# Performance work log

Hardware: AMD Instinct MI355X
Metric: run time of the kernel (lower is better)

Reference implementation:

```python
import jax, jax.numpy as jnp
import numpy as np


def layer_norm(x, gamma, beta, eps=1e-6):
    # Torch module uses unbiased std (ddof=1) and divides by (std + eps)
    mean = x.mean(-1, keepdims=True)
    std = jnp.std(x, axis=-1, keepdims=True, ddof=1)
    return gamma * (x - mean) / (std + eps) + beta


def gelu_erf(x):
    return 0.5 * x * (1.0 + jax.lax.erf(x / jnp.sqrt(jnp.asarray(2.0, x.dtype))))


def setup_inputs() -> dict:
    B, S, D, H, F = 32, 512, 1024, 16, 4096
    key = jax.random.key(0)
    ks = jax.random.split(key, 16)
    w = lambda k, shp: (jax.random.normal(k, shp, jnp.float32) * 0.02)
    return {
        "x": jax.random.normal(ks[0], (B, S, D), jnp.float32),
        "mask": jax.random.randint(ks[1], (B, S), 0, 2).astype(jnp.int32),
        "adj": jax.random.normal(ks[2], (B, 1, S, S), jnp.float32) * 0.1,
        "num_head": H,
        "Wq": w(ks[3], (D, D)), "bq": jnp.zeros((D,), jnp.float32),
        "Wk": w(ks[4], (D, D)), "bk": jnp.zeros((D,), jnp.float32),
        "Wv": w(ks[5], (D, D)), "bv": jnp.zeros((D,), jnp.float32),
        "Wo": w(ks[6], (D, D)), "bo": jnp.zeros((D,), jnp.float32),
        "W1": w(ks[7], (D, F)), "b1": jnp.zeros((F,), jnp.float32),
        "W2": w(ks[8], (F, D)), "b2": jnp.zeros((D,), jnp.float32),
        "gamma": jnp.ones((D,), jnp.float32),
        "beta": jnp.zeros((D,), jnp.float32),
    }


def reference(x, mask, adj, num_head, Wq, bq, Wk, bk, Wv, bv, Wo, bo,
              W1, b1, W2, b2, gamma, beta):
    B, S, D = x.shape
    H = num_head
    dk = D // H
    split = lambda t: t.reshape(B, S, H, dk).transpose(0, 2, 1, 3)  # [B,H,S,dk]
    q = split(x @ Wq + bq)
    k = split(x @ Wk + bk)
    v = split(x @ Wv + bv)
    scores = jnp.einsum('bhqd,bhkd->bhqk', q, k) / np.float32(np.sqrt(dk))
    m = mask[:, None, None, :].astype(x.dtype)  # [B,1,1,S]
    scores = scores + m * jnp.asarray(-1e9, x.dtype) + adj
    attn = jax.nn.softmax(scores, axis=-1)
    ctx = jnp.einsum('bhqk,bhkd->bhqd', attn, v)
    ctx = ctx.transpose(0, 2, 1, 3).reshape(B, S, D)
    attn_out = ctx @ Wo + bo  # dropout is identity at eval
    out1 = layer_norm(x + attn_out, gamma, beta)
    ffn = gelu_erf(out1 @ W1 + b1) @ W2 + b2
    return layer_norm(out1 + ffn, gamma, beta)
```

## Files before the change

### kernel.cpp

```cpp
#include <hip/hip_runtime.h>
#include <stdint.h>
#include <math.h>

typedef unsigned short u16;
typedef __attribute__((ext_vector_type(8))) __bf16 bf16x8;
typedef __attribute__((ext_vector_type(4))) float f32x4;
typedef __attribute__((ext_vector_type(4))) unsigned short u16x4;

__device__ __forceinline__ float b2f(u16 u) {
    unsigned int i = ((unsigned int)u) << 16;
    float f; __builtin_memcpy(&f, &i, 4); return f;
}
__device__ __forceinline__ u16 f2b(float f) {
    unsigned int i; __builtin_memcpy(&i, &f, 4);
    i = (i + 0x7FFFu + ((i >> 16) & 1u)) >> 16;
    return (u16)i;
}
__device__ __forceinline__ bf16x8 ld8_cvt(const float* p) {
    float4 f0 = *(const float4*)p, f1 = *(const float4*)(p + 4);
    u16 t[8] = {f2b(f0.x), f2b(f0.y), f2b(f0.z), f2b(f0.w),
                f2b(f1.x), f2b(f1.y), f2b(f1.z), f2b(f1.w)};
    bf16x8 r; __builtin_memcpy(&r, t, 16); return r;
}

__global__ __launch_bounds__(256) void transpose_f32_bf16(
    const float* __restrict__ in, u16* __restrict__ out, int R, int C)
{
    __shared__ float t[32][33];
    int bx = blockIdx.x * 32, by = blockIdx.y * 32;
    int x = threadIdx.x, y = threadIdx.y;
    #pragma unroll
    for (int j = 0; j < 32; j += 8)
        t[y + j][x] = in[(size_t)(by + y + j) * C + bx + x];
    __syncthreads();
    #pragma unroll
    for (int j = 0; j < 32; j += 8)
        out[(size_t)(bx + y + j) * R + by + x] = f2b(t[x][y + j]);
}

template<int EPI, bool AF32>
__global__ __launch_bounds__(256) void gemm_bt(
    const void* __restrict__ Av, const u16* __restrict__ Bt, int N, int K,
    u16* __restrict__ C, const float* __restrict__ bias,
    u16* __restrict__ qo, u16* __restrict__ ko, u16* __restrict__ vo,
    const float* __restrict__ bq, const float* __restrict__ bk,
    const float* __restrict__ bv)
{
    __shared__ __align__(16) u16 Asm[128 * 32];
    __shared__ __align__(16) u16 Bsm[128 * 32];
    const int tid  = threadIdx.x;
    const int lane = tid & 63, wave = tid >> 6;
    const int lrow = lane & 15, quad = lane >> 4;
    const int bm = blockIdx.x * 128, bn = blockIdx.y * 128;

    const int srow = tid >> 2;
    const int skol = (tid & 3) * 8;
    const float* gAf0 = (const float*)Av + (size_t)(bm + srow) * K + skol;
    const float* gAf1 = gAf0 + (size_t)64 * K;
    const u16*   gAh0 = (const u16*)Av + (size_t)(bm + srow) * K + skol;
    const u16*   gAh1 = gAh0 + (size_t)64 * K;
    const u16*   gB0  = Bt + (size_t)(bn + srow) * K + skol;
    const u16*   gB1  = gB0 + (size_t)64 * K;

    bf16x8 ra0, ra1, rb0, rb1;
    if (AF32) { ra0 = ld8_cvt(gAf0); ra1 = ld8_cvt(gAf1); }
    else      { ra0 = *(const bf16x8*)gAh0; ra1 = *(const bf16x8*)gAh1; }
    rb0 = *(const bf16x8*)gB0;
    rb1 = *(const bf16x8*)gB1;

    const int wm = wave >> 1, wn = wave & 1;
    f32x4 acc[4][4] = {};

    for (int kt = 0; kt < K; kt += 32) {
        __syncthreads();
        *(bf16x8*)&Asm[(size_t)tid * 8]         = ra0;
        *(bf16x8*)&Asm[((size_t)tid + 256) * 8] = ra1;
        *(bf16x8*)&Bsm[(size_t)tid * 8]         = rb0;
        *(bf16x8*)&Bsm[((size_t)tid + 256) * 8] = rb1;
        __syncthreads();

        if (kt + 32 < K) {
            if (AF32) { ra0 = ld8_cvt(gAf0 + kt + 32); ra1 = ld8_cvt(gAf1 + kt + 32); }
            else      { ra0 = *(const bf16x8*)(gAh0 + kt + 32);
                        ra1 = *(const bf16x8*)(gAh1 + kt + 32); }
            rb0 = *(const bf16x8*)(gB0 + kt + 32);
            rb1 = *(const bf16x8*)(gB1 + kt + 32);
        }

        bf16x8 af[4], bf[4];
        #pragma unroll
        for (int mt = 0; mt < 4; mt++)
            af[mt] = *(const bf16x8*)&Asm[(wm * 64 + mt * 16 + lrow) * 32 + quad * 8];
        #pragma unroll
        for (int nt = 0; nt < 4; nt++)
            bf[nt] = *(const bf16x8*)&Bsm[(wn * 64 + nt * 16 + lrow) * 32 + quad * 8];
        #pragma unroll
        for (int mt = 0; mt < 4; mt++)
            #pragma unroll
            for (int nt = 0; nt < 4; nt++)
                acc[mt][nt] = __builtin_amdgcn_mfma_f32_16x16x32_bf16(
                    af[mt], bf[nt], acc[mt][nt], 0, 0, 0);
    }

    #pragma unroll
    for (int nt = 0; nt < 4; nt++) {
        int col = bn + wn * 64 + nt * 16 + lrow;
        int mat = 0, hh = 0, dd = 0;
        float bval;
        if (EPI == 2) {
            mat  = col >> 10; int dcol = col & 1023;
            hh = dcol >> 6;   dd = dcol & 63;
            const float* bp = (mat == 0) ? bq : ((mat == 1) ? bk : bv);
            bval = bp[dcol];
        } else {
            bval = bias[col];
        }
        #pragma unroll
        for (int mt = 0; mt < 4; mt++) {
            #pragma unroll
            for (int r = 0; r < 4; r++) {
                int row = bm + wm * 64 + mt * 16 + quad * 4 + r;
                float v = acc[mt][nt][r] + bval;
                if (EPI == 1) v = 0.5f * v * (1.0f + erff(v * 0.70710678118654752f));
                if (EPI == 2) {
                    int b = row >> 9, s = row & 511;
                    u16* dst = (mat == 0) ? qo : ((mat == 1) ? ko : vo);
                    dst[(((size_t)(b * 16 + hh)) * 512 + s) * 64 + dd] = f2b(v);
                } else {
                    C[(size_t)row * N + col] = f2b(v);
                }
            }
        }
    }
}

__global__ __launch_bounds__(256) void attn_kernel(
    const u16* __restrict__ Q, const u16* __restrict__ Kb, const u16* __restrict__ Vb,
    const float* __restrict__ adj, const int* __restrict__ mask, u16* __restrict__ ctx)
{
    const int S = 512, H = 16;
    __shared__ __align__(16) u16 Ksm[32 * 64];
    __shared__ __align__(16) u16 Vt [64 * 32];
    __shared__ __align__(16) u16 Psm[4][16 * 32];

    int tid = threadIdx.x, lane = tid & 63, wave = tid >> 6;
    int lrow = lane & 15, quad = lane >> 4;
    int qt = blockIdx.x, h = blockIdx.y, b = blockIdx.z;

    size_t headoff = ((size_t)(b * H + h)) * S * 64;
    const u16* qp = Q + headoff;
    const u16* kp = Kb + headoff;
    const u16* vp = Vb + headoff;
    const float* adjb = adj + (size_t)b * S * S;
    const int* maskb = mask + b * S;
    int q0 = qt * 64 + wave * 16;

    bf16x8 qf0 = *(const bf16x8*)(qp + (size_t)(q0 + lrow) * 64 + quad * 8);
    bf16x8 qf1 = *(const bf16x8*)(qp + (size_t)(q0 + lrow) * 64 + 32 + quad * 8);

    float m_run[4] = {-1e30f, -1e30f, -1e30f, -1e30f};
    float l_run[4] = {0.f, 0.f, 0.f, 0.f};
    f32x4 o[4] = {};

    int str = tid >> 3;
    int stc = (tid & 7) * 8;

    for (int kt = 0; kt < S; kt += 32) {
        __syncthreads();
        *(bf16x8*)&Ksm[str * 64 + stc] = *(const bf16x8*)(kp + (size_t)(kt + str) * 64 + stc);
        {
            bf16x8 vv = *(const bf16x8*)(vp + (size_t)(kt + str) * 64 + stc);
            const u16* tv = (const u16*)&vv;
            #pragma unroll
            for (int j = 0; j < 8; j++) Vt[(stc + j) * 32 + str] = tv[j];
        }
        __syncthreads();

        f32x4 sc[2];
        #pragma unroll
        for (int f = 0; f < 2; f++) {
            f32x4 cf = {};
            bf16x8 kf0 = *(const bf16x8*)&Ksm[(f * 16 + lrow) * 64 + quad * 8];
            bf16x8 kf1 = *(const bf16x8*)&Ksm[(f * 16 + lrow) * 64 + 32 + quad * 8];
            cf = __builtin_amdgcn_mfma_f32_16x16x32_bf16(qf0, kf0, cf, 0, 0, 0);
            cf = __builtin_amdgcn_mfma_f32_16x16x32_bf16(qf1, kf1, cf, 0, 0, 0);
            int key = kt + f * 16 + lrow;
            float mterm = maskb[key] ? -1e9f : 0.0f;
            #pragma unroll
            for (int r = 0; r < 4; r++) {
                int qrow = q0 + quad * 4 + r;
                sc[f][r] = cf[r] * 0.125f + mterm + adjb[(size_t)qrow * S + key];
            }
        }

        float mx[4], al[4], sm[4];
        #pragma unroll
        for (int r = 0; r < 4; r++) mx[r] = fmaxf(sc[0][r], sc[1][r]);
        #pragma unroll
        for (int mk = 1; mk < 16; mk <<= 1)
            #pragma unroll
            for (int r = 0; r < 4; r++) mx[r] = fmaxf(mx[r], __shfl_xor(mx[r], mk));
        #pragma unroll
        for (int r = 0; r < 4; r++) {
            float mn = fmaxf(m_run[r], mx[r]);
            al[r] = __expf(fminf(m_run[r] - mn, 0.f));
            m_run[r] = mn;
        }
        #pragma unroll
        for (int f = 0; f < 2; f++)
            #pragma unroll
            for (int r = 0; r < 4; r++)
                sc[f][r] = __expf(fminf(sc[f][r] - m_run[r], 0.f));
        #pragma unroll
        for (int r = 0; r < 4; r++) sm[r] = sc[0][r] + sc[1][r];
        #pragma unroll
        for (int mk = 1; mk < 16; mk <<= 1)
            #pragma unroll
            for (int r = 0; r < 4; r++) sm[r] += __shfl_xor(sm[r], mk);
        #pragma unroll
        for (int r = 0; r < 4; r++) l_run[r] = l_run[r] * al[r] + sm[r];
        #pragma unroll
        for (int nt = 0; nt < 4; nt++)
            #pragma unroll
            for (int r = 0; r < 4; r++) o[nt][r] *= al[r];

        #pragma unroll
        for (int f = 0; f < 2; f++)
            #pragma unroll
            for (int r = 0; r < 4; r++)
                Psm[wave][(quad * 4 + r) * 32 + f * 16 + lrow] = f2b(sc[f][r]);
        bf16x8 pa = *(const bf16x8*)&Psm[wave][lrow * 32 + quad * 8];
        #pragma unroll
        for (int nt = 0; nt < 4; nt++) {
            bf16x8 vf = *(const bf16x8*)&Vt[(nt * 16 + lrow) * 32 + quad * 8];
            o[nt] = __builtin_amdgcn_mfma_f32_16x16x32_bf16(pa, vf, o[nt], 0, 0, 0);
        }
    }

    #pragma unroll
    for (int nt = 0; nt < 4; nt++)
        #pragma unroll
        for (int r = 0; r < 4; r++) {
            int qrow = q0 + quad * 4 + r;
            ctx[((size_t)b * 512 + qrow) * 1024 + h * 64 + nt * 16 + lrow] =
                f2b(o[nt][r] / l_run[r]);
        }
}

template<int MODE>
__global__ __launch_bounds__(256) void add_ln(
    const void* __restrict__ Xv, const void* __restrict__ Yv,
    const float* __restrict__ gamma, const float* __restrict__ beta,
    void* __restrict__ outv)
{
    const int D = 1024;
    int row = blockIdx.x, tid = threadIdx.x;
    int lane = tid & 63, wave = tid >> 6;
    size_t base = (size_t)row * D + tid * 4;

    float x[4];
    if (MODE == 0) {
        float4 xf = *(const float4*)((const float*)Xv + base);
        u16x4  uy = *(const u16x4*)((const u16*)Yv + base);
        x[0] = xf.x + b2f(uy[0]); x[1] = xf.y + b2f(uy[1]);
        x[2] = xf.z + b2f(uy[2]); x[3] = xf.w + b2f(uy[3]);
    } else {
        u16x4 ux = *(const u16x4*)((const u16*)Xv + base);
        u16x4 uy = *(const u16x4*)((const u16*)Yv + base);
        #pragma unroll
        for (int j = 0; j < 4; j++) x[j] = b2f(ux[j]) + b2f(uy[j]);
    }

    float s = x[0] + x[1] + x[2] + x[3];
    #pragma unroll
    for (int mk = 1; mk < 64; mk <<= 1) s += __shfl_xor(s, mk);
    __shared__ float red[8];
    if (lane == 0) red[wave] = s;
    __syncthreads();
    float mean = (red[0] + red[1] + red[2] + red[3]) * (1.0f / 1024.0f);

    float c[4], q = 0.f;
    #pragma unroll
    for (int j = 0; j < 4; j++) { c[j] = x[j] - mean; q += c[j] * c[j]; }
    #pragma unroll
    for (int mk = 1; mk < 64; mk <<= 1) q += __shfl_xor(q, mk);
    if (lane == 0) red[4 + wave] = q;
    __syncthreads();
    float var = (red[4] + red[5] + red[6] + red[7]) * (1.0f / 1023.0f);
    float inv = 1.0f / (sqrtf(var) + 1e-6f);

    float4 g4 = *(const float4*)(gamma + tid * 4);
    float4 b4 = *(const float4*)(beta + tid * 4);
    float gv[4] = {g4.x, g4.y, g4.z, g4.w};
    float bv[4] = {b4.x, b4.y, b4.z, b4.w};
    if (MODE == 0) {
        u16x4 ov;
        #pragma unroll
        for (int j = 0; j < 4; j++) ov[j] = f2b(gv[j] * c[j] * inv + bv[j]);
        *(u16x4*)((u16*)outv + base) = ov;
    } else {
        float4 ov;
        ov.x = gv[0] * c[0] * inv + bv[0];
        ov.y = gv[1] * c[1] * inv + bv[1];
        ov.z = gv[2] * c[2] * inv + bv[2];
        ov.w = gv[3] * c[3] * inv + bv[3];
        *(float4*)((float*)outv + base) = ov;
    }
}

extern "C" void kernel_launch(void* const* d_in, const int* in_sizes, int n_in,
                              void* d_out, int out_size, void* d_ws, size_t ws_size,
                              hipStream_t stream)
{
    const float* x    = (const float*)d_in[0];
    const int*   mask = (const int*)d_in[1];
    const float* adj  = (const float*)d_in[2];
    const float* Wq = (const float*)d_in[4];  const float* bq = (const float*)d_in[5];
    const float* Wk = (const float*)d_in[6];  const float* bk = (const float*)d_in[7];
    const float* Wv = (const float*)d_in[8];  const float* bv = (const float*)d_in[9];
    const float* Wo = (const float*)d_in[10]; const float* bo = (const float*)d_in[11];
    const float* W1 = (const float*)d_in[12]; const float* b1 = (const float*)d_in[13];
    const float* W2 = (const float*)d_in[14]; const float* b2 = (const float*)d_in[15];
    const float* gamma = (const float*)d_in[16];
    const float* beta  = (const float*)d_in[17];
    float* out = (float*)d_out;

    const size_t MB = 1024ull * 1024;
    char* w = (char*)d_ws;
    u16* Wqkv_t = (u16*)(w + 0 * MB);
    u16* Wo_t   = (u16*)(w + 6 * MB);
    u16* W1_t   = (u16*)(w + 8 * MB);
    u16* W2_t   = (u16*)(w + 16 * MB);
    u16* out1   = (u16*)(w + 24 * MB);
    u16* qg     = (u16*)(w + 56 * MB);
    u16* kg     = (u16*)(w + 64 * MB);
    u16* vg     = (u16*)(w + 72 * MB);
    u16* ctxg   = (u16*)(w + 80 * MB);
    u16* aog    = (u16*)(w + 88 * MB);
    u16* hid    = (u16*)(w + 56 * MB);
    u16* ffn    = (u16*)(w + 88 * MB);

    dim3 tb(32, 8);
    transpose_f32_bf16<<<dim3(32, 32),  tb, 0, stream>>>(Wq, Wqkv_t,                1024, 1024);
    transpose_f32_bf16<<<dim3(32, 32),  tb, 0, stream>>>(Wk, Wqkv_t + 1024ull*1024, 1024, 1024);
    transpose_f32_bf16<<<dim3(32, 32),  tb, 0, stream>>>(Wv, Wqkv_t + 2048ull*1024, 1024, 1024);
    transpose_f32_bf16<<<dim3(32, 32),  tb, 0, stream>>>(Wo, Wo_t,                  1024, 1024);
    transpose_f32_bf16<<<dim3(128, 32), tb, 0, stream>>>(W1, W1_t,                  1024, 4096);
    transpose_f32_bf16<<<dim3(32, 128), tb, 0, stream>>>(W2, W2_t,                  4096, 1024);

    for (int g = 0; g < 4; g++) {
        const float* xg = x + (size_t)g * 4096 * 1024;
        gemm_bt<2, true><<<dim3(32, 24), 256, 0, stream>>>(xg, Wqkv_t, 3072, 1024,
            nullptr, nullptr, qg, kg, vg, bq, bk, bv);
        attn_kernel<<<dim3(8, 16, 8), 256, 0, stream>>>(qg, kg, vg,
            adj + (size_t)g * 8 * 512 * 512, mask + g * 8 * 512, ctxg);
        gemm_bt<0, false><<<dim3(32, 8), 256, 0, stream>>>(ctxg, Wo_t, 1024, 1024,
            aog, bo, nullptr, nullptr, nullptr, nullptr, nullptr, nullptr);
        add_ln<0><<<4096, 256, 0, stream>>>(xg, aog, gamma, beta,
            out1 + (size_t)g * 4096 * 1024);
    }

    for (int c = 0; c < 4; c++) {
        const u16* o1c = out1 + (size_t)c * 4096 * 1024;
        gemm_bt<1, false><<<dim3(32, 32), 256, 0, stream>>>(o1c, W1_t, 4096, 1024,
            hid, b1, nullptr, nullptr, nullptr, nullptr, nullptr, nullptr);
        gemm_bt<0, false><<<dim3(32, 8), 256, 0, stream>>>(hid, W2_t, 1024, 4096,
            ffn, b2, nullptr, nullptr, nullptr, nullptr, nullptr, nullptr);
        add_ln<1><<<4096, 256, 0, stream>>>(o1c, ffn, gamma, beta,
            out + (size_t)c * 4096 * 1024);
    }
}
```

Baseline: 1.242 ms.

## Use direct global-to-LDS loads in GEMM and restructure FFN into K-split accumulation

The GEMM now loads tiles straight into LDS with global_load_lds and drops the register prefetch double-buffer. The input is pre-converted to bf16 by a separate kernel instead of being converted inside the GEMM. The Wo projection and first layernorm run once over all batches rather than per group. The FFN is split along the hidden dimension into four chunks, with W2 partial products accumulated in fp32 in the output buffer. This removes the staging registers and some launches, but loses load/compute overlap and adds read-modify-write traffic on the fp32 output.

```diff
diff --git a/kernel.cpp b/kernel.cpp
--- a/kernel.cpp
+++ b/kernel.cpp
@@ -22,6 +22,11 @@
                 f2b(f1.x), f2b(f1.y), f2b(f1.z), f2b(f1.w)};
     bf16x8 r; __builtin_memcpy(&r, t, 16); return r;
 }
+__device__ __forceinline__ void gl2lds16(const u16* g, u16* l) {
+    __builtin_amdgcn_global_load_lds(
+        (const __attribute__((address_space(1))) unsigned int*)g,
+        (__attribute__((address_space(3))) unsigned int*)l, 16, 0, 0);
+}
 
 __global__ __launch_bounds__(256) void transpose_f32_bf16(
     const float* __restrict__ in, u16* __restrict__ out, int R, int C)
@@ -38,10 +43,18 @@
         out[(size_t)(bx + y + j) * R + by + x] = f2b(t[x][y + j]);
 }
 
-template<int EPI, bool AF32>
+__global__ __launch_bounds__(256) void convert_f32_bf16(
+    const float* __restrict__ in, u16* __restrict__ out)
+{
+    size_t off = ((size_t)blockIdx.x * 256 + threadIdx.x) * 8;
+    *(bf16x8*)(out + off) = ld8_cvt(in + off);
+}
+
+template<int EPI, bool FIRST>
 __global__ __launch_bounds__(256) void gemm_bt(
-    const void* __restrict__ Av, const u16* __restrict__ Bt, int N, int K,
-    u16* __restrict__ C, const float* __restrict__ bias,
+    const u16* __restrict__ A, int lda, const u16* __restrict__ Bt, int ldb,
+    int N, int K, int ldc,
+    u16* __restrict__ C, float* __restrict__ Cf, const float* __restrict__ bias,
     u16* __restrict__ qo, u16* __restrict__ ko, u16* __restrict__ vo,
     const float* __restrict__ bq, const float* __restrict__ bk,
     const float* __restrict__ bv)
@@ -53,39 +66,26 @@
     const int lrow = lane & 15, quad = lane >> 4;
     const int bm = blockIdx.x * 128, bn = blockIdx.y * 128;
 
-    const int srow = tid >> 2;
-    const int skol = (tid & 3) * 8;
-    const float* gAf0 = (const float*)Av + (size_t)(bm + srow) * K + skol;
-    const float* gAf1 = gAf0 + (size_t)64 * K;
-    const u16*   gAh0 = (const u16*)Av + (size_t)(bm + srow) * K + skol;
-    const u16*   gAh1 = gAh0 + (size_t)64 * K;
-    const u16*   gB0  = Bt + (size_t)(bn + srow) * K + skol;
-    const u16*   gB1  = gB0 + (size_t)64 * K;
-
-    bf16x8 ra0, ra1, rb0, rb1;
-    if (AF32) { ra0 = ld8_cvt(gAf0); ra1 = ld8_cvt(gAf1); }
-    else      { ra0 = *(const bf16x8*)gAh0; ra1 = *(const bf16x8*)gAh1; }
-    rb0 = *(const bf16x8*)gB0;
-    rb1 = *(const bf16x8*)gB1;
+    const int c0   = wave * 2;
+    const int sub  = lane >> 2;
+    const int kcol = (lane & 3) * 8;
+    const u16* gA0 = A  + (size_t)(bm + c0 * 16 + sub)      * lda + kcol;
+    const u16* gA1 = A  + (size_t)(bm + c0 * 16 + 16 + sub) * lda + kcol;
+    const u16* gB0 = Bt + (size_t)(bn + c0 * 16 + sub)      * ldb + kcol;
+    const u16* gB1 = Bt + (size_t)(bn + c0 * 16 + 16 + sub) * ldb + kcol;
+    u16* lA0 = &Asm[c0 * 512]; u16* lA1 = &Asm[(c0 + 1) * 512];
+    u16* lB0 = &Bsm[c0 * 512]; u16* lB1 = &Bsm[(c0 + 1) * 512];
 
     const int wm = wave >> 1, wn = wave & 1;
     f32x4 acc[4][4] = {};
 
     for (int kt = 0; kt < K; kt += 32) {
         __syncthreads();
-        *(bf16x8*)&Asm[(size_t)tid * 8]         = ra0;
-        *(bf16x8*)&Asm[((size_t)tid + 256) * 8] = ra1;
-        *(bf16x8*)&Bsm[(size_t)tid * 8]         = rb0;
-        *(bf16x8*)&Bsm[((size_t)tid + 256) * 8] = rb1;
+        gl2lds16(gA0 + kt, lA0);
+        gl2lds16(gA1 + kt, lA1);
+        gl2lds16(gB0 + kt, lB0);
+        gl2lds16(gB1 + kt, lB1);
         __syncthreads();
-
-        if (kt + 32 < K) {
-            if (AF32) { ra0 = ld8_cvt(gAf0 + kt + 32); ra1 = ld8_cvt(gAf1 + kt + 32); }
-            else      { ra0 = *(const bf16x8*)(gAh0 + kt + 32);
-                        ra1 = *(const bf16x8*)(gAh1 + kt + 32); }
-            rb0 = *(const bf16x8*)(gB0 + kt + 32);
-            rb1 = *(const bf16x8*)(gB1 + kt + 32);
-        }
 
         bf16x8 af[4], bf[4];
         #pragma unroll
@@ -106,13 +106,13 @@
     for (int nt = 0; nt < 4; nt++) {
         int col = bn + wn * 64 + nt * 16 + lrow;
         int mat = 0, hh = 0, dd = 0;
-        float bval;
+        float bval = 0.f;
         if (EPI == 2) {
             mat  = col >> 10; int dcol = col & 1023;
             hh = dcol >> 6;   dd = dcol & 63;
             const float* bp = (mat == 0) ? bq : ((mat == 1) ? bk : bv);
             bval = bp[dcol];
-        } else {
+        } else if (EPI != 3 || FIRST) {
             bval = bias[col];
         }
         #pragma unroll
@@ -120,14 +120,20 @@
             #pragma unroll
             for (int r = 0; r < 4; r++) {
                 int row = bm + wm * 64 + mt * 16 + quad * 4 + r;
-                float v = acc[mt][nt][r] + bval;
-                if (EPI == 1) v = 0.5f * v * (1.0f + erff(v * 0.70710678118654752f));
-                if (EPI == 2) {
-                    int b = row >> 9, s = row & 511;
-                    u16* dst = (mat == 0) ? qo : ((mat == 1) ? ko : vo);
-                    dst[(((size_t)(b * 16 + hh)) * 512 + s) * 64 + dd] = f2b(v);
+                if (EPI == 3) {
+                    size_t idx = (size_t)row * ldc + col;
+                    float v = acc[mt][nt][r] + (FIRST ? bval : Cf[idx]);
+                    Cf[idx] = v;
                 } else {
-                    C[(size_t)row * N + col] = f2b(v);
+                    float v = acc[mt][nt][r] + bval;
+                    if (EPI == 1) v = 0.5f * v * (1.0f + erff(v * 0.70710678118654752f));
+                    if (EPI == 2) {
+                        int b = row >> 9, s = row & 511;
+                        u16* dst = (mat == 0) ? qo : ((mat == 1) ? ko : vo);
+                        dst[(((size_t)(b * 16 + hh)) * 512 + s) * 64 + dd] = f2b(v);
+                    } else {
+                        C[(size_t)row * ldc + col] = f2b(v);
+                    }
                 }
             }
         }
@@ -265,10 +271,10 @@
         x[0] = xf.x + b2f(uy[0]); x[1] = xf.y + b2f(uy[1]);
         x[2] = xf.z + b2f(uy[2]); x[3] = xf.w + b2f(uy[3]);
     } else {
-        u16x4 ux = *(const u16x4*)((const u16*)Xv + base);
-        u16x4 uy = *(const u16x4*)((const u16*)Yv + base);
-        #pragma unroll
-        for (int j = 0; j < 4; j++) x[j] = b2f(ux[j]) + b2f(uy[j]);
+        u16x4  ux = *(const u16x4*)((const u16*)Xv + base);
+        float4 yf = *(const float4*)((const float*)Yv + base);
+        x[0] = b2f(ux[0]) + yf.x; x[1] = b2f(ux[1]) + yf.y;
+        x[2] = b2f(ux[2]) + yf.z; x[3] = b2f(ux[3]) + yf.w;
     }
 
     float s = x[0] + x[1] + x[2] + x[3];
@@ -292,18 +298,18 @@
     float4 g4 = *(const float4*)(gamma + tid * 4);
     float4 b4 = *(const float4*)(beta + tid * 4);
     float gv[4] = {g4.x, g4.y, g4.z, g4.w};
-    float bv[4] = {b4.x, b4.y, b4.z, b4.w};
+    float bb[4] = {b4.x, b4.y, b4.z, b4.w};
     if (MODE == 0) {
         u16x4 ov;
         #pragma unroll
-        for (int j = 0; j < 4; j++) ov[j] = f2b(gv[j] * c[j] * inv + bv[j]);
+        for (int j = 0; j < 4; j++) ov[j] = f2b(gv[j] * c[j] * inv + bb[j]);
         *(u16x4*)((u16*)outv + base) = ov;
     } else {
         float4 ov;
-        ov.x = gv[0] * c[0] * inv + bv[0];
-        ov.y = gv[1] * c[1] * inv + bv[1];
-        ov.z = gv[2] * c[2] * inv + bv[2];
-        ov.w = gv[3] * c[3] * inv + bv[3];
+        ov.x = gv[0] * c[0] * inv + bb[0];
+        ov.y = gv[1] * c[1] * inv + bb[1];
+        ov.z = gv[2] * c[2] * inv + bb[2];
+        ov.w = gv[3] * c[3] * inv + bb[3];
         *(float4*)((float*)outv + base) = ov;
     }
 }
@@ -331,14 +337,14 @@
     u16* Wo_t   = (u16*)(w + 6 * MB);
     u16* W1_t   = (u16*)(w + 8 * MB);
     u16* W2_t   = (u16*)(w + 16 * MB);
+    u16* ctxall = (u16*)(w + 24 * MB);
     u16* out1   = (u16*)(w + 24 * MB);
-    u16* qg     = (u16*)(w + 56 * MB);
-    u16* kg     = (u16*)(w + 64 * MB);
-    u16* vg     = (u16*)(w + 72 * MB);
-    u16* ctxg   = (u16*)(w + 80 * MB);
-    u16* aog    = (u16*)(w + 88 * MB);
+    u16* xb     = (u16*)(w + 56 * MB);
+    u16* qg     = (u16*)(w + 64 * MB);
+    u16* kg     = (u16*)(w + 72 * MB);
+    u16* vg     = (u16*)(w + 80 * MB);
+    u16* aog    = (u16*)(w + 56 * MB);
     u16* hid    = (u16*)(w + 56 * MB);
-    u16* ffn    = (u16*)(w + 88 * MB);
 
     dim3 tb(32, 8);
     transpose_f32_bf16<<<dim3(32, 32),  tb, 0, stream>>>(Wq, Wqkv_t,                1024, 1024);
@@ -350,23 +356,34 @@
 
     for (int g = 0; g < 4; g++) {
         const float* xg = x + (size_t)g * 4096 * 1024;
-        gemm_bt<2, true><<<dim3(32, 24), 256, 0, stream>>>(xg, Wqkv_t, 3072, 1024,
-            nullptr, nullptr, qg, kg, vg, bq, bk, bv);
+        convert_f32_bf16<<<2048, 256, 0, stream>>>(xg, xb);
+        gemm_bt<2, false><<<dim3(32, 24), 256, 0, stream>>>(
+            xb, 1024, Wqkv_t, 1024, 3072, 1024, 0,
+            nullptr, nullptr, nullptr, qg, kg, vg, bq, bk, bv);
         attn_kernel<<<dim3(8, 16, 8), 256, 0, stream>>>(qg, kg, vg,
-            adj + (size_t)g * 8 * 512 * 512, mask + g * 8 * 512, ctxg);
-        gemm_bt<0, false><<<dim3(32, 8), 256, 0, stream>>>(ctxg, Wo_t, 1024, 1024,
-            aog, bo, nullptr, nullptr, nullptr, nullptr, nullptr, nullptr);
-        add_ln<0><<<4096, 256, 0, stream>>>(xg, aog, gamma, beta,
-            out1 + (size_t)g * 4096 * 1024);
-    }
+            adj + (size_t)g * 8 * 512 * 512, mask + g * 8 * 512,
+            ctxall + (size_t)g * 4096 * 1024);
+    }
+
+    gemm_bt<0, false><<<dim3(128, 8), 256, 0, stream>>>(
+        ctxall, 1024, Wo_t, 1024, 1024, 1024, 1024,
+        aog, nullptr, bo, nullptr, nullptr, nullptr, nullptr, nullptr, nullptr);
+    add_ln<0><<<16384, 256, 0, stream>>>(x, aog, gamma, beta, out1);
 
     for (int c = 0; c < 4; c++) {
-        const u16* o1c = out1 + (size_t)c * 4096 * 1024;
-        gemm_bt<1, false><<<dim3(32, 32), 256, 0, stream>>>(o1c, W1_t, 4096, 1024,
-            hid, b1, nullptr, nullptr, nullptr, nullptr, nullptr, nullptr);
-        gemm_bt<0, false><<<dim3(32, 8), 256, 0, stream>>>(hid, W2_t, 1024, 4096,
-            ffn, b2, nullptr, nullptr, nullptr, nullptr, nullptr, nullptr);
-        add_ln<1><<<4096, 256, 0, stream>>>(o1c, ffn, gamma, beta,
-            out + (size_t)c * 4096 * 1024);
-    }
-}
+        gemm_bt<1, false><<<dim3(128, 8), 256, 0, stream>>>(
+            out1, 1024, W1_t + (size_t)c * 1024 * 1024, 1024, 1024, 1024, 1024,
+            hid, nullptr, b1 + c * 1024,
+            nullptr, nullptr, nullptr, nullptr, nullptr, nullptr);
+        if (c == 0)
+            gemm_bt<3, true><<<dim3(128, 8), 256, 0, stream>>>(
+                hid, 1024, W2_t + (size_t)c * 1024, 4096, 1024, 1024, 1024,
+                nullptr, out, b2, nullptr, nullptr, nullptr, nullptr, nullptr, nullptr);
+        else
+            gemm_bt<3, false><<<dim3(128, 8), 256, 0, stream>>>(
+                hid, 1024, W2_t + (size_t)c * 1024, 4096, 1024, 1024, 1024,
+                nullptr, out, b2, nullptr, nullptr, nullptr, nullptr, nullptr, nullptr);
+    }
+
+    add_ln<1><<<16384, 256, 0, stream>>>(out1, out, gamma, beta, out);
+}
```

Result: slower. 1.308 ms (+5.3%).
